# Kernel optimization log

Measured on AMD Instinct MI355X. Metric: run time of the kernel, lower is better.

The kernel has to match this reference:

```python
import jax, jax.numpy as jnp
import numpy as np

N_NODES = 20000   # len(pert2id)
N_EDGES = 400000  # top_20 graph: ~20 edges/node
BATCH   = 4096
IN_DIM  = 64
HID_DIM = 128
OUT_DIM = 64
HEADS   = 2
HEAD_D  = HID_DIM // HEADS  # 64 (also OUT_DIM per head on last layer)


def setup_inputs() -> dict:
    key = jax.random.key(0)
    ks = jax.random.split(key, 24)
    inp = {
        "pert_indices": jax.random.randint(ks[0], (BATCH,), 0, N_NODES),
        "edge_index": jax.random.randint(ks[1], (2, N_EDGES), 0, N_NODES),
        "edge_weight": jax.random.uniform(ks[2], (N_EDGES,), dtype=jnp.float32),
        "emb": jax.random.normal(ks[3], (N_NODES, IN_DIM), dtype=jnp.float32) * 0.02,
    }
    # 4 GATv2 layers: layer0 IN->HEADS*HEAD_D (concat), layers 1,2 HID->HEADS*HEAD_D (concat),
    # layer3 HID->HEADS*OUT_DIM (mean over heads -> OUT_DIM)
    in_dims = [IN_DIM, HID_DIM, HID_DIM, HID_DIM]
    concat = [True, True, True, False]
    k = 4
    for i in range(4):
        d_in = in_dims[i]
        d_head = HEAD_D
        sc = 1.0 / np.sqrt(d_in)
        inp[f"Wl{i}"] = jax.random.normal(ks[k], (d_in, HEADS * d_head), dtype=jnp.float32) * sc; k += 1
        inp[f"Wr{i}"] = jax.random.normal(ks[k], (d_in, HEADS * d_head), dtype=jnp.float32) * sc; k += 1
        inp[f"a{i}"]  = jax.random.normal(ks[k], (HEADS, d_head), dtype=jnp.float32) * (1.0 / np.sqrt(d_head)); k += 1
        out_dim = HEADS * d_head if concat[i] else d_head
        inp[f"b{i}"]  = jnp.zeros((out_dim,), dtype=jnp.float32); k += 1
    return inp


def _gatv2_layer(x, src, dst, ew, Wl, Wr, a, b, concat):
    N = x.shape[0]
    H, D = a.shape
    xl = (x @ Wl).reshape(N, H, D)   # source transform (messages)
    xr = (x @ Wr).reshape(N, H, D)   # target transform
    # GATv2 score: a^T LeakyReLU(Wl x_j + Wr x_i) per edge, per head -> [E, H]
    e = jnp.einsum("ehd,hd->eh", jax.nn.leaky_relu(xl[src] + xr[dst], 0.2), a)
    # segment softmax over incoming edges of each target node
    m = jax.ops.segment_max(e, dst, num_segments=N)
    m = jnp.where(jnp.isfinite(m), m, 0.0)  # isolated nodes
    ex = jnp.exp(e - m[dst])
    s = jax.ops.segment_sum(ex, dst, num_segments=N)
    alpha = ex / (s[dst] + 1e-16)            # [E, H]
    msg = (alpha * ew[:, None])[:, :, None] * xl[src]  # edge-weighted messages [E,H,D]
    out = jax.ops.segment_sum(msg, dst, num_segments=N)  # [N,H,D]
    out = out.reshape(N, H * D) if concat else out.mean(axis=1)
    return out + b


def reference(pert_indices, edge_index, edge_weight, emb,
              Wl0, Wr0, a0, b0, Wl1, Wr1, a1, b1,
              Wl2, Wr2, a2, b2, Wl3, Wr3, a3, b3):
    src, dst = edge_index[0], edge_index[1]
    layers = [(Wl0, Wr0, a0, b0, True), (Wl1, Wr1, a1, b1, True),
              (Wl2, Wr2, a2, b2, True), (Wl3, Wr3, a3, b3, False)]
    x = emb
    for i, (Wl, Wr, a, b, cc) in enumerate(layers):
        x = _gatv2_layer(x, src, dst, edge_weight, Wl, Wr, a, b, cc)
        if i < len(layers) - 1:
            x = jax.nn.elu(x)
    # node_emb[pert_indices]
    return x[pert_indices]
```

## Files before the change

kernel.cpp:

```cpp
#include <hip/hip_runtime.h>
#include <math.h>

#define N_NODES 20000
#define N_EDGES 400000
#define BATCH   4096
#define MTILES  (N_NODES / 16)

typedef __attribute__((ext_vector_type(8))) short short8v;
typedef __attribute__((ext_vector_type(4))) float f32x4;

__device__ __forceinline__ void bf16split(float v, short& h, short& l)
{
    unsigned u  = __float_as_uint(v);
    unsigned hu = u & 0xFFFF0000u;
    h = (short)(hu >> 16);
    const float lo = v - __uint_as_float(hu);
    l = (short)(__float_as_uint(lo) >> 16);
}

template<int K>
__global__ __launch_bounds__(256)
void pack_x_kernel(const float* __restrict__ x, short* __restrict__ xpk)
{
    constexpr int KB = K / 32;
    const int t = blockIdx.x * 256 + threadIdx.x;
    if (t >= MTILES * KB * 64) return;
    const int lane  = t & 63;
    const int kb    = (t >> 6) % KB;
    const int mtile = t / (64 * KB);
    const int node  = mtile * 16 + (lane & 15);
    const int k0    = kb * 32 + (lane >> 4) * 8;
    const float* xp = x + (size_t)node * K + k0;
    short8v h, l;
#pragma unroll
    for (int e = 0; e < 8; ++e) {
        short hh, ll; bf16split(xp[e], hh, ll);
        h[e] = hh; l[e] = ll;
    }
    short* ob = xpk + ((size_t)(mtile * KB + kb) * 2) * 512 + lane * 8;
    *(short8v*)ob         = h;
    *(short8v*)(ob + 512) = l;
}

template<int K>
__global__ __launch_bounds__(256)
void pack_w_kernel(const float* __restrict__ Wl, const float* __restrict__ Wr,
                   short* __restrict__ wpk)
{
    constexpr int KB = K / 32;
    const int t = blockIdx.x * 256 + threadIdx.x;
    if (t >= 16 * KB * 64) return;
    const int lane = t & 63;
    const int kb   = (t >> 6) % KB;
    const int nt   = t / (64 * KB);
    const float* W = (nt < 8) ? Wl : Wr;
    const int col  = (nt & 7) * 16 + (lane & 15);
    const int k0   = kb * 32 + (lane >> 4) * 8;
    short8v h, l;
#pragma unroll
    for (int e = 0; e < 8; ++e) {
        short hh, ll; bf16split(W[(size_t)(k0 + e) * 128 + col], hh, ll);
        h[e] = hh; l[e] = ll;
    }
    short* ob = wpk + ((size_t)(nt * KB + kb) * 2) * 512 + lane * 8;
    *(short8v*)ob         = h;
    *(short8v*)(ob + 512) = l;
}

template<int KB, int NWAVES>
__global__ __launch_bounds__(NWAVES * 64)
void mfma_transform_kernel(const short* __restrict__ xpk,
                           const short* __restrict__ wpk,
                           float* __restrict__ xl, float* __restrict__ xr)
{
    const int mtile = blockIdx.x;
    const int wid   = threadIdx.x >> 6;
    const int lane  = threadIdx.x & 63;

    short8v ah[KB], al[KB];
    const short* ab = xpk + ((size_t)mtile * KB * 2) * 512 + lane * 8;
#pragma unroll
    for (int kb = 0; kb < KB; ++kb) {
        ah[kb] = *(const short8v*)(ab + (size_t)(kb * 2 + 0) * 512);
        al[kb] = *(const short8v*)(ab + (size_t)(kb * 2 + 1) * 512);
    }

#pragma unroll
    for (int i = 0; i < 4; ++i) {
        const int nt = wid * 4 + i;
        const short* bb = wpk + ((size_t)nt * KB * 2) * 512 + lane * 8;
        f32x4 acc = {0.f, 0.f, 0.f, 0.f};
#pragma unroll
        for (int kb = 0; kb < KB; ++kb) {
            const short8v bh = *(const short8v*)(bb + (size_t)(kb * 2 + 0) * 512);
            const short8v bl = *(const short8v*)(bb + (size_t)(kb * 2 + 1) * 512);
            acc = __builtin_amdgcn_mfma_f32_16x16x32_bf16(ah[kb], bh, acc, 0, 0, 0);
            acc = __builtin_amdgcn_mfma_f32_16x16x32_bf16(ah[kb], bl, acc, 0, 0, 0);
            acc = __builtin_amdgcn_mfma_f32_16x16x32_bf16(al[kb], bh, acc, 0, 0, 0);
        }
        float* out = (nt < 8) ? xl : xr;
        const int colb = (nt & 7) * 16 + (lane & 15);
        const int row0 = mtile * 16 + (lane >> 4) * 4;
#pragma unroll
        for (int r = 0; r < 4; ++r)
            out[(size_t)(row0 + r) * 128 + colb] = acc[r];
    }
}

template<int K, int G>
__global__ __launch_bounds__(128)
void transform_r_pert_kernel(const float* __restrict__ x,
                             const int* __restrict__ pert,
                             const float* __restrict__ W,
                             float* __restrict__ out)
{
    const int t  = threadIdx.x;
    const int i0 = blockIdx.x * G;

    const float* __restrict__ xrow[G];
#pragma unroll
    for (int g = 0; g < G; ++g)
        xrow[g] = x + (size_t)pert[i0 + g] * K;

    float acc[G];
#pragma unroll
    for (int g = 0; g < G; ++g) acc[g] = 0.f;

    float4 xA[G], xB[G];
    float wA[4], wB[4];

    auto loadc = [&](float4* xs, float* w, int k) {
#pragma unroll
        for (int g = 0; g < G; ++g)
            xs[g] = *(const float4*)(xrow[g] + k);
#pragma unroll
        for (int u = 0; u < 4; ++u) w[u] = W[(k + u) * 128 + t];
    };
    auto fmac = [&](const float4* xs, const float* w) {
#pragma unroll
        for (int g = 0; g < G; ++g) {
            acc[g] = fmaf(xs[g].x, w[0], acc[g]);
            acc[g] = fmaf(xs[g].y, w[1], acc[g]);
            acc[g] = fmaf(xs[g].z, w[2], acc[g]);
            acc[g] = fmaf(xs[g].w, w[3], acc[g]);
        }
    };

    loadc(xA, wA, 0);
    for (int k0 = 0; k0 < K; k0 += 8) {
        if (k0 + 4 < K) loadc(xB, wB, k0 + 4);
        fmac(xA, wA);
        if (k0 + 8 < K) loadc(xA, wA, k0 + 8);
        fmac(xB, wB);
    }

#pragma unroll
    for (int g = 0; g < G; ++g)
        out[(size_t)(i0 + g) * 128 + t] = acc[g];
}

__global__ __launch_bounds__(256)
void zero_kernel(int* __restrict__ p, int n)
{
    const int i = blockIdx.x * blockDim.x + threadIdx.x;
    if (i < n) p[i] = 0;
}

__global__ __launch_bounds__(256)
void count_deg_kernel(const int* __restrict__ dst, int* __restrict__ deg, int E)
{
    const int e = blockIdx.x * blockDim.x + threadIdx.x;
    if (e < E) atomicAdd(&deg[dst[e]], 1);
}

#define CHUNK 20
#define SCAN_PAD (1024 * CHUNK)
__global__ __launch_bounds__(1024)
void scan_kernel(const int* __restrict__ deg, int* __restrict__ off,
                 int* __restrict__ cursor)
{
    __shared__ int xs[SCAN_PAD];
    __shared__ int sums[1024];
    const int t = threadIdx.x;
    for (int i = t; i < SCAN_PAD; i += 1024)
        xs[i] = (i < N_NODES) ? deg[i] : 0;
    __syncthreads();

    const int base = t * CHUNK;
    int local[CHUNK];
    int s = 0;
#pragma unroll
    for (int i = 0; i < CHUNK; ++i) {
        local[i] = s;
        s += xs[base + i];
    }
    sums[t] = s;
    __syncthreads();
    for (int d = 1; d < 1024; d <<= 1) {
        int v = (t >= d) ? sums[t - d] : 0;
        __syncthreads();
        sums[t] += v;
        __syncthreads();
    }
    const int prev = (t == 0) ? 0 : sums[t - 1];
#pragma unroll
    for (int i = 0; i < CHUNK; ++i)
        xs[base + i] = prev + local[i];
    __syncthreads();
    for (int i = t; i < N_NODES; i += 1024) {
        const int o = xs[i];
        off[i] = o;
        cursor[i] = o;
    }
    if (t == 1023) off[N_NODES] = sums[1023];
}

__global__ __launch_bounds__(256)
void scatter_kernel(const int* __restrict__ src, const int* __restrict__ dst,
                    const float* __restrict__ ew, int* __restrict__ cursor,
                    int* __restrict__ ssrc, float* __restrict__ sew, int E)
{
    const int e = blockIdx.x * blockDim.x + threadIdx.x;
    if (e >= E) return;
    const int p = atomicAdd(&cursor[dst[e]], 1);
    ssrc[p] = src[e];
    sew[p]  = ew[e];
}

template<int LAST>
__global__ __launch_bounds__(256)
void gat_node_kernel(const float* __restrict__ xl, const float* __restrict__ xr,
                     const int* __restrict__ off, const int* __restrict__ ssrc,
                     const float* __restrict__ sew, const float* __restrict__ a,
                     const float* __restrict__ b, float* __restrict__ xout,
                     const int* __restrict__ nodemap, int nnodes)
{
    const int widx = (int)((blockIdx.x * blockDim.x + threadIdx.x) >> 6);
    if (widx >= nnodes) return;
    const int node = LAST ? nodemap[widx] : widx;
    const int xrrow = widx;
    const int lane = threadIdx.x & 63;
    const int q  = lane >> 4;
    const int h  = (lane >> 3) & 1;
    const int j  = lane & 7;
    const int cb = h * 64 + j * 8;

    const float4 xrA = *(const float4*)(xr + (size_t)xrrow * 128 + cb);
    const float4 xrB = *(const float4*)(xr + (size_t)xrrow * 128 + cb + 4);
    const float4 aA  = *(const float4*)(a + cb);
    const float4 aB  = *(const float4*)(a + cb + 4);

    const int e0 = off[node], e1 = off[node + 1];

    float m = -1e30f, s = 0.f;
    float acc[8];
#pragma unroll
    for (int k = 0; k < 8; ++k) acc[k] = 0.f;

    for (int ebase = e0; ebase < e1; ebase += 4) {
        const int  ei    = ebase + q;
        const bool valid = ei < e1;
        const int  eic   = valid ? ei : (e1 - 1);
        const int  sn    = ssrc[eic];
        const float w    = valid ? sew[eic] : 0.f;
        const float4 xA = *(const float4*)(xl + (size_t)sn * 128 + cb);
        const float4 xB = *(const float4*)(xl + (size_t)sn * 128 + cb + 4);

        float v0 = xA.x + xrA.x, v1 = xA.y + xrA.y;
        float v2 = xA.z + xrA.z, v3 = xA.w + xrA.w;
        float v4 = xB.x + xrB.x, v5 = xB.y + xrB.y;
        float v6 = xB.z + xrB.z, v7 = xB.w + xrB.w;
        v0 = fmaxf(v0, 0.2f * v0); v1 = fmaxf(v1, 0.2f * v1);
        v2 = fmaxf(v2, 0.2f * v2); v3 = fmaxf(v3, 0.2f * v3);
        v4 = fmaxf(v4, 0.2f * v4); v5 = fmaxf(v5, 0.2f * v5);
        v6 = fmaxf(v6, 0.2f * v6); v7 = fmaxf(v7, 0.2f * v7);
        float t0 = fmaf(v0, aA.x, v1 * aA.y);
        float t1 = fmaf(v2, aA.z, v3 * aA.w);
        float t2 = fmaf(v4, aB.x, v5 * aB.y);
        float t3 = fmaf(v6, aB.z, v7 * aB.w);
        float p = (t0 + t1) + (t2 + t3);
        p += __shfl_xor(p, 1, 64);
        p += __shfl_xor(p, 2, 64);
        p += __shfl_xor(p, 4, 64);
        p = valid ? p : -1e30f;

        const float d   = p - m;
        const float t   = __expf(-fabsf(d));
        const bool  pos = d > 0.f;
        const float r   = pos ? t : 1.f;
        const float ex  = pos ? 1.f : t;
        m = pos ? p : m;
        const float c = ex * w;
        s = s * r + ex;
        acc[0] = acc[0] * r + c * xA.x;
        acc[1] = acc[1] * r + c * xA.y;
        acc[2] = acc[2] * r + c * xA.z;
        acc[3] = acc[3] * r + c * xA.w;
        acc[4] = acc[4] * r + c * xB.x;
        acc[5] = acc[5] * r + c * xB.y;
        acc[6] = acc[6] * r + c * xB.z;
        acc[7] = acc[7] * r + c * xB.w;
    }

    float mg = fmaxf(m, __shfl_xor(m, 16, 64));
    mg = fmaxf(mg, __shfl_xor(mg, 32, 64));
    const float rq = __expf(m - mg);
    float sq = s * rq;
    sq += __shfl_xor(sq, 16, 64);
    sq += __shfl_xor(sq, 32, 64);
#pragma unroll
    for (int k = 0; k < 8; ++k) {
        float v = acc[k] * rq;
        v += __shfl_xor(v, 16, 64);
        v += __shfl_xor(v, 32, 64);
        acc[k] = v;
    }
    const float inv = 1.f / (sq + 1e-16f);

    if (!LAST) {
        if (q == 0) {
            float o[8];
#pragma unroll
            for (int k = 0; k < 8; ++k) {
                float u = acc[k] * inv + b[cb + k];
                o[k] = u > 0.f ? u : expm1f(u);
            }
            *(float4*)(xout + (size_t)node * 128 + cb)     = make_float4(o[0], o[1], o[2], o[3]);
            *(float4*)(xout + (size_t)node * 128 + cb + 4) = make_float4(o[4], o[5], o[6], o[7]);
        }
    } else {
        float o[8];
#pragma unroll
        for (int k = 0; k < 8; ++k) {
            const float v = acc[k] * inv;
            o[k] = 0.5f * (v + __shfl_xor(v, 8, 64)) + b[j * 8 + k];
        }
        if (q == 0 && h == 0) {
            *(float4*)(xout + (size_t)widx * 64 + j * 8)     = make_float4(o[0], o[1], o[2], o[3]);
            *(float4*)(xout + (size_t)widx * 64 + j * 8 + 4) = make_float4(o[4], o[5], o[6], o[7]);
        }
    }
}

extern "C" void kernel_launch(void* const* d_in, const int* in_sizes, int n_in,
                              void* d_out, int out_size, void* d_ws, size_t ws_size,
                              hipStream_t stream)
{
    const int*   pert = (const int*)d_in[0];
    const int*   eidx = (const int*)d_in[1];
    const float* ew   = (const float*)d_in[2];
    const float* emb  = (const float*)d_in[3];
    const float* Wl[4] = {(const float*)d_in[4],  (const float*)d_in[8],
                          (const float*)d_in[12], (const float*)d_in[16]};
    const float* Wr[4] = {(const float*)d_in[5],  (const float*)d_in[9],
                          (const float*)d_in[13], (const float*)d_in[17]};
    const float* av[4] = {(const float*)d_in[6],  (const float*)d_in[10],
                          (const float*)d_in[14], (const float*)d_in[18]};
    const float* bv[4] = {(const float*)d_in[7],  (const float*)d_in[11],
                          (const float*)d_in[15], (const float*)d_in[19]};

    const int N = N_NODES, E = N_EDGES;
    const int* srcp = eidx;
    const int* dstp = eidx + E;

    float* ws   = (float*)d_ws;
    float* xbuf = ws;
    float* xl   = xbuf + (size_t)N * 128;
    float* xr   = xl   + (size_t)N * 128;
    short* xpk  = (short*)(xr + (size_t)N * 128);
    short* wpk  = xpk + (size_t)MTILES * 4 * 2 * 512;
    int*   deg  = (int*)(wpk + 4 * 65536);
    int*   off  = deg + N;
    int*   cur  = off + N + 1;
    int*   ssrc = cur + N;
    float* sew  = (float*)(ssrc + E);

    zero_kernel<<<(N + 255) / 256, 256, 0, stream>>>(deg, N);
    count_deg_kernel<<<(E + 255) / 256, 256, 0, stream>>>(dstp, deg, E);
    scan_kernel<<<1, 1024, 0, stream>>>(deg, off, cur);
    scatter_kernel<<<(E + 255) / 256, 256, 0, stream>>>(srcp, dstp, ew, cur,
                                                        ssrc, sew, E);

    pack_w_kernel<64><<<8,  256, 0, stream>>>(Wl[0], Wr[0], wpk);
    pack_w_kernel<128><<<16, 256, 0, stream>>>(Wl[1], Wr[1], wpk + 1 * 65536);
    pack_w_kernel<128><<<16, 256, 0, stream>>>(Wl[2], Wr[2], wpk + 2 * 65536);
    pack_w_kernel<128><<<16, 256, 0, stream>>>(Wl[3], Wr[3], wpk + 3 * 65536);

    pack_x_kernel<64><<<MTILES * 2 * 64 / 256, 256, 0, stream>>>(emb, xpk);
    mfma_transform_kernel<2, 4><<<MTILES, 256, 0, stream>>>(xpk, wpk, xl, xr);
    gat_node_kernel<0><<<(N * 64 + 255) / 256, 256, 0, stream>>>(
        xl, xr, off, ssrc, sew, av[0], bv[0], xbuf, nullptr, N);

    for (int layer = 1; layer < 3; ++layer) {
        pack_x_kernel<128><<<MTILES * 4 * 64 / 256, 256, 0, stream>>>(xbuf, xpk);
        mfma_transform_kernel<4, 4><<<MTILES, 256, 0, stream>>>(
            xpk, wpk + layer * 65536, xl, xr);
        gat_node_kernel<0><<<(N * 64 + 255) / 256, 256, 0, stream>>>(
            xl, xr, off, ssrc, sew, av[layer], bv[layer], xbuf, nullptr, N);
    }

    pack_x_kernel<128><<<MTILES * 4 * 64 / 256, 256, 0, stream>>>(xbuf, xpk);
    mfma_transform_kernel<4, 2><<<MTILES, 128, 0, stream>>>(
        xpk, wpk + 3 * 65536, xl, xr);
    transform_r_pert_kernel<128, 8><<<BATCH / 8, 128, 0, stream>>>(
        xbuf, pert, Wr[3], xr);
    gat_node_kernel<1><<<(BATCH * 64 + 255) / 256, 256, 0, stream>>>(
        xl, xr, off, ssrc, sew, av[3], bv[3], (float*)d_out, pert, BATCH);
}
```

Measured before the change: 277.2 us.

## Fuse bf16 split packing into MFMA transform and widen GAT edge parallelism

Removes the separate pack_x kernel: the transform kernel now stages the fp32 activation tile in LDS and performs the hi/lo bf16 split in registers before the MFMAs. This drops one launch per layer and a round trip of the packed buffer through global memory. Separately, the GAT node kernel is restructured so each lane handles both heads, eight edges per wave iteration instead of four, with per-head online softmax state. That halves loop iterations per node but doubles register state and loads per lane.

```diff
diff --git a/kernel.cpp b/kernel.cpp
--- a/kernel.cpp
+++ b/kernel.cpp
@@ -16,30 +16,6 @@
     h = (short)(hu >> 16);
     const float lo = v - __uint_as_float(hu);
     l = (short)(__float_as_uint(lo) >> 16);
-}
-
-template<int K>
-__global__ __launch_bounds__(256)
-void pack_x_kernel(const float* __restrict__ x, short* __restrict__ xpk)
-{
-    constexpr int KB = K / 32;
-    const int t = blockIdx.x * 256 + threadIdx.x;
-    if (t >= MTILES * KB * 64) return;
-    const int lane  = t & 63;
-    const int kb    = (t >> 6) % KB;
-    const int mtile = t / (64 * KB);
-    const int node  = mtile * 16 + (lane & 15);
-    const int k0    = kb * 32 + (lane >> 4) * 8;
-    const float* xp = x + (size_t)node * K + k0;
-    short8v h, l;
-#pragma unroll
-    for (int e = 0; e < 8; ++e) {
-        short hh, ll; bf16split(xp[e], hh, ll);
-        h[e] = hh; l[e] = ll;
-    }
-    short* ob = xpk + ((size_t)(mtile * KB + kb) * 2) * 512 + lane * 8;
-    *(short8v*)ob         = h;
-    *(short8v*)(ob + 512) = l;
 }
 
 template<int K>
@@ -69,20 +45,40 @@
 
 template<int KB, int NWAVES>
 __global__ __launch_bounds__(NWAVES * 64)
-void mfma_transform_kernel(const short* __restrict__ xpk,
+void mfma_transform_kernel(const float* __restrict__ x,
                            const short* __restrict__ wpk,
                            float* __restrict__ xl, float* __restrict__ xr)
 {
+    constexpr int K  = KB * 32;
+    constexpr int KP = K + 4;
+    __shared__ float xs[16 * KP];
     const int mtile = blockIdx.x;
     const int wid   = threadIdx.x >> 6;
     const int lane  = threadIdx.x & 63;
 
+    {
+        const float4* __restrict__ src = (const float4*)(x + (size_t)mtile * 16 * K);
+        for (int idx = threadIdx.x; idx < 16 * K / 4; idx += NWAVES * 64) {
+            const int row = idx / (K / 4), c4 = idx % (K / 4);
+            *(float4*)(xs + row * KP + c4 * 4) = src[idx];
+        }
+    }
+    __syncthreads();
+
     short8v ah[KB], al[KB];
-    const short* ab = xpk + ((size_t)mtile * KB * 2) * 512 + lane * 8;
-#pragma unroll
-    for (int kb = 0; kb < KB; ++kb) {
-        ah[kb] = *(const short8v*)(ab + (size_t)(kb * 2 + 0) * 512);
-        al[kb] = *(const short8v*)(ab + (size_t)(kb * 2 + 1) * 512);
+    {
+        const float* ab = xs + (lane & 15) * KP + (lane >> 4) * 8;
+#pragma unroll
+        for (int kb = 0; kb < KB; ++kb) {
+            const float4 f0 = *(const float4*)(ab + kb * 32);
+            const float4 f1 = *(const float4*)(ab + kb * 32 + 4);
+            float tmp[8] = {f0.x, f0.y, f0.z, f0.w, f1.x, f1.y, f1.z, f1.w};
+#pragma unroll
+            for (int e = 0; e < 8; ++e) {
+                short hh, ll; bf16split(tmp[e], hh, ll);
+                ah[kb][e] = hh; al[kb][e] = ll;
+            }
+        }
     }
 
 #pragma unroll
@@ -240,105 +236,147 @@
     const int node = LAST ? nodemap[widx] : widx;
     const int xrrow = widx;
     const int lane = threadIdx.x & 63;
-    const int q  = lane >> 4;
-    const int h  = (lane >> 3) & 1;
+    const int q  = lane >> 3;
     const int j  = lane & 7;
-    const int cb = h * 64 + j * 8;
-
-    const float4 xrA = *(const float4*)(xr + (size_t)xrrow * 128 + cb);
-    const float4 xrB = *(const float4*)(xr + (size_t)xrrow * 128 + cb + 4);
-    const float4 aA  = *(const float4*)(a + cb);
-    const float4 aB  = *(const float4*)(a + cb + 4);
+    const int c0 = j * 8;
+
+    const float* xrp = xr + (size_t)xrrow * 128;
+    const float4 r0 = *(const float4*)(xrp + c0);
+    const float4 r1 = *(const float4*)(xrp + c0 + 4);
+    const float4 r2 = *(const float4*)(xrp + c0 + 64);
+    const float4 r3 = *(const float4*)(xrp + c0 + 68);
+    const float4 a0 = *(const float4*)(a + c0);
+    const float4 a1 = *(const float4*)(a + c0 + 4);
+    const float4 a2 = *(const float4*)(a + c0 + 64);
+    const float4 a3 = *(const float4*)(a + c0 + 68);
 
     const int e0 = off[node], e1 = off[node + 1];
 
-    float m = -1e30f, s = 0.f;
-    float acc[8];
-#pragma unroll
-    for (int k = 0; k < 8; ++k) acc[k] = 0.f;
-
-    for (int ebase = e0; ebase < e1; ebase += 4) {
+    float m0 = -1e30f, m1 = -1e30f, s0 = 0.f, s1 = 0.f;
+    float4 acc0 = {0,0,0,0}, acc1 = {0,0,0,0}, acc2 = {0,0,0,0}, acc3 = {0,0,0,0};
+
+    auto lrelu4 = [](float4 v) {
+        v.x = fmaxf(v.x, 0.2f * v.x); v.y = fmaxf(v.y, 0.2f * v.y);
+        v.z = fmaxf(v.z, 0.2f * v.z); v.w = fmaxf(v.w, 0.2f * v.w);
+        return v;
+    };
+    auto dot4 = [](float4 u, float4 v) {
+        return fmaf(u.x, v.x, fmaf(u.y, v.y, fmaf(u.z, v.z, u.w * v.w)));
+    };
+    auto upd4 = [](float4 acc, float r, float c, float4 xv) {
+        acc.x = fmaf(c, xv.x, acc.x * r); acc.y = fmaf(c, xv.y, acc.y * r);
+        acc.z = fmaf(c, xv.z, acc.z * r); acc.w = fmaf(c, xv.w, acc.w * r);
+        return acc;
+    };
+
+    for (int ebase = e0; ebase < e1; ebase += 8) {
         const int  ei    = ebase + q;
         const bool valid = ei < e1;
         const int  eic   = valid ? ei : (e1 - 1);
         const int  sn    = ssrc[eic];
         const float w    = valid ? sew[eic] : 0.f;
-        const float4 xA = *(const float4*)(xl + (size_t)sn * 128 + cb);
-        const float4 xB = *(const float4*)(xl + (size_t)sn * 128 + cb + 4);
-
-        float v0 = xA.x + xrA.x, v1 = xA.y + xrA.y;
-        float v2 = xA.z + xrA.z, v3 = xA.w + xrA.w;
-        float v4 = xB.x + xrB.x, v5 = xB.y + xrB.y;
-        float v6 = xB.z + xrB.z, v7 = xB.w + xrB.w;
-        v0 = fmaxf(v0, 0.2f * v0); v1 = fmaxf(v1, 0.2f * v1);
-        v2 = fmaxf(v2, 0.2f * v2); v3 = fmaxf(v3, 0.2f * v3);
-        v4 = fmaxf(v4, 0.2f * v4); v5 = fmaxf(v5, 0.2f * v5);
-        v6 = fmaxf(v6, 0.2f * v6); v7 = fmaxf(v7, 0.2f * v7);
-        float t0 = fmaf(v0, aA.x, v1 * aA.y);
-        float t1 = fmaf(v2, aA.z, v3 * aA.w);
-        float t2 = fmaf(v4, aB.x, v5 * aB.y);
-        float t3 = fmaf(v6, aB.z, v7 * aB.w);
-        float p = (t0 + t1) + (t2 + t3);
-        p += __shfl_xor(p, 1, 64);
-        p += __shfl_xor(p, 2, 64);
-        p += __shfl_xor(p, 4, 64);
-        p = valid ? p : -1e30f;
-
-        const float d   = p - m;
-        const float t   = __expf(-fabsf(d));
-        const bool  pos = d > 0.f;
-        const float r   = pos ? t : 1.f;
-        const float ex  = pos ? 1.f : t;
-        m = pos ? p : m;
-        const float c = ex * w;
-        s = s * r + ex;
-        acc[0] = acc[0] * r + c * xA.x;
-        acc[1] = acc[1] * r + c * xA.y;
-        acc[2] = acc[2] * r + c * xA.z;
-        acc[3] = acc[3] * r + c * xA.w;
-        acc[4] = acc[4] * r + c * xB.x;
-        acc[5] = acc[5] * r + c * xB.y;
-        acc[6] = acc[6] * r + c * xB.z;
-        acc[7] = acc[7] * r + c * xB.w;
-    }
-
-    float mg = fmaxf(m, __shfl_xor(m, 16, 64));
-    mg = fmaxf(mg, __shfl_xor(mg, 32, 64));
-    const float rq = __expf(m - mg);
-    float sq = s * rq;
-    sq += __shfl_xor(sq, 16, 64);
-    sq += __shfl_xor(sq, 32, 64);
-#pragma unroll
-    for (int k = 0; k < 8; ++k) {
-        float v = acc[k] * rq;
+        const float* xp  = xl + (size_t)sn * 128;
+        const float4 x0 = *(const float4*)(xp + c0);
+        const float4 x1 = *(const float4*)(xp + c0 + 4);
+        const float4 x2 = *(const float4*)(xp + c0 + 64);
+        const float4 x3 = *(const float4*)(xp + c0 + 68);
+
+        const float4 v0 = lrelu4(make_float4(x0.x + r0.x, x0.y + r0.y, x0.z + r0.z, x0.w + r0.w));
+        const float4 v1 = lrelu4(make_float4(x1.x + r1.x, x1.y + r1.y, x1.z + r1.z, x1.w + r1.w));
+        const float4 v2 = lrelu4(make_float4(x2.x + r2.x, x2.y + r2.y, x2.z + r2.z, x2.w + r2.w));
+        const float4 v3 = lrelu4(make_float4(x3.x + r3.x, x3.y + r3.y, x3.z + r3.z, x3.w + r3.w));
+
+        float p0 = dot4(v0, a0) + dot4(v1, a1);
+        float p1 = dot4(v2, a2) + dot4(v3, a3);
+        p0 += __shfl_xor(p0, 1, 64); p1 += __shfl_xor(p1, 1, 64);
+        p0 += __shfl_xor(p0, 2, 64); p1 += __shfl_xor(p1, 2, 64);
+        p0 += __shfl_xor(p0, 4, 64); p1 += __shfl_xor(p1, 4, 64);
+        p0 = valid ? p0 : -1e30f;
+        p1 = valid ? p1 : -1e30f;
+
+        {
+            const float d   = p0 - m0;
+            const float t   = __expf(-fabsf(d));
+            const bool  pos = d > 0.f;
+            const float r   = pos ? t : 1.f;
+            const float ex  = pos ? 1.f : t;
+            m0 = pos ? p0 : m0;
+            const float c = ex * w;
+            s0 = s0 * r + ex;
+            acc0 = upd4(acc0, r, c, x0);
+            acc1 = upd4(acc1, r, c, x1);
+        }
+        {
+            const float d   = p1 - m1;
+            const float t   = __expf(-fabsf(d));
+            const bool  pos = d > 0.f;
+            const float r   = pos ? t : 1.f;
+            const float ex  = pos ? 1.f : t;
+            m1 = pos ? p1 : m1;
+            const float c = ex * w;
+            s1 = s1 * r + ex;
+            acc2 = upd4(acc2, r, c, x2);
+            acc3 = upd4(acc3, r, c, x3);
+        }
+    }
+
+    auto redmax = [](float v) {
+        v = fmaxf(v, __shfl_xor(v, 8, 64));
+        v = fmaxf(v, __shfl_xor(v, 16, 64));
+        return fmaxf(v, __shfl_xor(v, 32, 64));
+    };
+    auto redsum = [](float v) {
+        v += __shfl_xor(v, 8, 64);
         v += __shfl_xor(v, 16, 64);
-        v += __shfl_xor(v, 32, 64);
-        acc[k] = v;
-    }
-    const float inv = 1.f / (sq + 1e-16f);
-
+        return v + __shfl_xor(v, 32, 64);
+    };
+    const float mg0 = redmax(m0), mg1 = redmax(m1);
+    const float rq0 = __expf(m0 - mg0), rq1 = __expf(m1 - mg1);
+    const float sq0 = redsum(s0 * rq0), sq1 = redsum(s1 * rq1);
+    auto redacc = [&](float4 acc, float rq) {
+        acc.x = redsum(acc.x * rq); acc.y = redsum(acc.y * rq);
+        acc.z = redsum(acc.z * rq); acc.w = redsum(acc.w * rq);
+        return acc;
+    };
+    acc0 = redacc(acc0, rq0); acc1 = redacc(acc1, rq0);
+    acc2 = redacc(acc2, rq1); acc3 = redacc(acc3, rq1);
+    const float inv0 = 1.f / (sq0 + 1e-16f);
+    const float inv1 = 1.f / (sq1 + 1e-16f);
+
+    if (q != 0) return;
     if (!LAST) {
-        if (q == 0) {
-            float o[8];
-#pragma unroll
-            for (int k = 0; k < 8; ++k) {
-                float u = acc[k] * inv + b[cb + k];
-                o[k] = u > 0.f ? u : expm1f(u);
-            }
-            *(float4*)(xout + (size_t)node * 128 + cb)     = make_float4(o[0], o[1], o[2], o[3]);
-            *(float4*)(xout + (size_t)node * 128 + cb + 4) = make_float4(o[4], o[5], o[6], o[7]);
-        }
+        const float4 b0 = *(const float4*)(b + c0);
+        const float4 b1 = *(const float4*)(b + c0 + 4);
+        const float4 b2 = *(const float4*)(b + c0 + 64);
+        const float4 b3 = *(const float4*)(b + c0 + 68);
+        auto fin = [](float4 acc, float inv, float4 bb) {
+            float4 o;
+            o.x = acc.x * inv + bb.x; o.x = o.x > 0.f ? o.x : expm1f(o.x);
+            o.y = acc.y * inv + bb.y; o.y = o.y > 0.f ? o.y : expm1f(o.y);
+            o.z = acc.z * inv + bb.z; o.z = o.z > 0.f ? o.z : expm1f(o.z);
+            o.w = acc.w * inv + bb.w; o.w = o.w > 0.f ? o.w : expm1f(o.w);
+            return o;
+        };
+        float* op = xout + (size_t)node * 128;
+        *(float4*)(op + c0)      = fin(acc0, inv0, b0);
+        *(float4*)(op + c0 + 4)  = fin(acc1, inv0, b1);
+        *(float4*)(op + c0 + 64) = fin(acc2, inv1, b2);
+        *(float4*)(op + c0 + 68) = fin(acc3, inv1, b3);
     } else {
-        float o[8];
-#pragma unroll
-        for (int k = 0; k < 8; ++k) {
-            const float v = acc[k] * inv;
-            o[k] = 0.5f * (v + __shfl_xor(v, 8, 64)) + b[j * 8 + k];
-        }
-        if (q == 0 && h == 0) {
-            *(float4*)(xout + (size_t)widx * 64 + j * 8)     = make_float4(o[0], o[1], o[2], o[3]);
-            *(float4*)(xout + (size_t)widx * 64 + j * 8 + 4) = make_float4(o[4], o[5], o[6], o[7]);
-        }
+        const float4 b0 = *(const float4*)(b + c0);
+        const float4 b1 = *(const float4*)(b + c0 + 4);
+        float4 o0, o1;
+        o0.x = 0.5f * (acc0.x * inv0 + acc2.x * inv1) + b0.x;
+        o0.y = 0.5f * (acc0.y * inv0 + acc2.y * inv1) + b0.y;
+        o0.z = 0.5f * (acc0.z * inv0 + acc2.z * inv1) + b0.z;
+        o0.w = 0.5f * (acc0.w * inv0 + acc2.w * inv1) + b0.w;
+        o1.x = 0.5f * (acc1.x * inv0 + acc3.x * inv1) + b1.x;
+        o1.y = 0.5f * (acc1.y * inv0 + acc3.y * inv1) + b1.y;
+        o1.z = 0.5f * (acc1.z * inv0 + acc3.z * inv1) + b1.z;
+        o1.w = 0.5f * (acc1.w * inv0 + acc3.w * inv1) + b1.w;
+        float* op = xout + (size_t)widx * 64;
+        *(float4*)(op + c0)     = o0;
+        *(float4*)(op + c0 + 4) = o1;
     }
 }
 
@@ -367,8 +405,7 @@
     float* xbuf = ws;
     float* xl   = xbuf + (size_t)N * 128;
     float* xr   = xl   + (size_t)N * 128;
-    short* xpk  = (short*)(xr + (size_t)N * 128);
-    short* wpk  = xpk + (size_t)MTILES * 4 * 2 * 512;
+    short* wpk  = (short*)(xr + (size_t)N * 128);
     int*   deg  = (int*)(wpk + 4 * 65536);
     int*   off  = deg + N;
     int*   cur  = off + N + 1;
@@ -386,22 +423,19 @@
     pack_w_kernel<128><<<16, 256, 0, stream>>>(Wl[2], Wr[2], wpk + 2 * 65536);
     pack_w_kernel<128><<<16, 256, 0, stream>>>(Wl[3], Wr[3], wpk + 3 * 65536);
 
-    pack_x_kernel<64><<<MTILES * 2 * 64 / 256, 256, 0, stream>>>(emb, xpk);
-    mfma_transform_kernel<2, 4><<<MTILES, 256, 0, stream>>>(xpk, wpk, xl, xr);
+    mfma_transform_kernel<2, 4><<<MTILES, 256, 0, stream>>>(emb, wpk, xl, xr);
     gat_node_kernel<0><<<(N * 64 + 255) / 256, 256, 0, stream>>>(
         xl, xr, off, ssrc, sew, av[0], bv[0], xbuf, nullptr, N);
 
     for (int layer = 1; layer < 3; ++layer) {
-        pack_x_kernel<128><<<MTILES * 4 * 64 / 256, 256, 0, stream>>>(xbuf, xpk);
         mfma_transform_kernel<4, 4><<<MTILES, 256, 0, stream>>>(
-            xpk, wpk + layer * 65536, xl, xr);
+            xbuf, wpk + layer * 65536, xl, xr);
         gat_node_kernel<0><<<(N * 64 + 255) / 256, 256, 0, stream>>>(
             xl, xr, off, ssrc, sew, av[layer], bv[layer], xbuf, nullptr, N);
     }
 
-    pack_x_kernel<128><<<MTILES * 4 * 64 / 256, 256, 0, stream>>>(xbuf, xpk);
     mfma_transform_kernel<4, 2><<<MTILES, 128, 0, stream>>>(
-        xpk, wpk + 3 * 65536, xl, xr);
+        xbuf, wpk + 3 * 65536, xl, xr);
     transform_r_pert_kernel<128, 8><<<BATCH / 8, 128, 0, stream>>>(
         xbuf, pert, Wr[3], xr);
     gat_node_kernel<1><<<(BATCH * 64 + 255) / 256, 256, 0, stream>>>(
```

Result: slower. 290.5 us (+4.8%).
